# Performance work log

Measured on AMD Instinct MI355X. Metric: run time of the kernel, lower is better.

## Reference

```python
import jax, jax.numpy as jnp
import numpy as np

N_NODES = 50000
N_EDGES = 800000
ATOM_DIM = 32
EDGE_DIM = 16
HIDDEN = 64
NUM_STEPS = 3
NUM_GRAPHS = 256
OUT_DIM = 1


def setup_inputs() -> dict:
    key = jax.random.key(0)
    ks = jax.random.split(key, 20)
    s = 0.05
    inp = {
        "x": jax.random.normal(ks[0], (N_NODES, ATOM_DIM), dtype=jnp.float32),
        "edge_index": jax.random.randint(ks[1], (2, N_EDGES), 0, N_NODES),
        "edge_attr": jax.random.normal(ks[2], (N_EDGES, EDGE_DIM), dtype=jnp.float32),
        "batch": jnp.sort(jax.random.randint(ks[3], (N_NODES,), 0, NUM_GRAPHS)),
        # atom embedding
        "W_embed": jax.random.normal(ks[4], (ATOM_DIM, HIDDEN)) * s,
        "b_embed": jnp.zeros((HIDDEN,)),
        # message MLP: Linear(2H+E, H) -> ReLU -> Linear(H, H)
        "W_m1": jax.random.normal(ks[5], (2 * HIDDEN + EDGE_DIM, HIDDEN)) * s,
        "b_m1": jnp.zeros((HIDDEN,)),
        "W_m2": jax.random.normal(ks[6], (HIDDEN, HIDDEN)) * s,
        "b_m2": jnp.zeros((HIDDEN,)),
        # GRUCell (torch layout: [3H, in] stacked r,z,n)
        "W_ih": jax.random.normal(ks[7], (3 * HIDDEN, HIDDEN)) * s,
        "b_ih": jnp.zeros((3 * HIDDEN,)),
        "W_hh": jax.random.normal(ks[8], (3 * HIDDEN, HIDDEN)) * s,
        "b_hh": jnp.zeros((3 * HIDDEN,)),
        # head: Linear(2H, H) -> ReLU -> Linear(H, out)
        "W_h1": jax.random.normal(ks[9], (2 * HIDDEN, HIDDEN)) * s,
        "b_h1": jnp.zeros((HIDDEN,)),
        "W_h2": jax.random.normal(ks[10], (HIDDEN, OUT_DIM)) * s,
        "b_h2": jnp.zeros((OUT_DIM,)),
    }
    return inp


def _gru_cell(inp, h, W_ih, b_ih, W_hh, b_hh):
    gi = inp @ W_ih.T + b_ih   # [N, 3H]
    gh = h @ W_hh.T + b_hh     # [N, 3H]
    i_r, i_z, i_n = jnp.split(gi, 3, axis=-1)
    h_r, h_z, h_n = jnp.split(gh, 3, axis=-1)
    r = jax.nn.sigmoid(i_r + h_r)
    z = jax.nn.sigmoid(i_z + h_z)
    n = jnp.tanh(i_n + r * h_n)
    return (1.0 - z) * n + z * h


def reference(x, edge_index, edge_attr, batch,
              W_embed, b_embed, W_m1, b_m1, W_m2, b_m2,
              W_ih, b_ih, W_hh, b_hh, W_h1, b_h1, W_h2, b_h2):
    h = x @ W_embed + b_embed                       # [N, H]
    src, dst = edge_index[0], edge_index[1]         # PyG: x_j = x[src], x_i = x[dst]
    for _ in range(NUM_STEPS):                      # tied weights
        m = jnp.concatenate([h[src], h[dst], edge_attr], axis=-1)  # [E, 2H+ED]
        m = jax.nn.relu(m @ W_m1 + b_m1) @ W_m2 + b_m2             # [E, H]
        agg = jax.ops.segment_sum(m, dst, num_segments=N_NODES)    # scatter-add
        h = _gru_cell(agg, h, W_ih, b_ih, W_hh, b_hh)
    g_sum = jax.ops.segment_sum(h, batch, num_segments=NUM_GRAPHS)  # [G, H]
    cnt = jax.ops.segment_sum(jnp.ones((N_NODES,), h.dtype), batch,
                              num_segments=NUM_GRAPHS)
    g_mean = g_sum / jnp.maximum(cnt, 1.0)[:, None]
    g = jnp.concatenate([g_sum, g_mean], axis=-1)   # [G, 2H]
    return jax.nn.relu(g @ W_h1 + b_h1) @ W_h2 + b_h2  # [G, out]
```

## Files before the change

kernel.cpp:

```cpp
#include <hip/hip_runtime.h>
#include <math.h>

#define NN 50000
#define NE 800000
#define AD 32
#define ED 16
#define HD 64
#define NG 256
#define NTILES (NE / 16)
#define EGRID 1024
#define TPX (NTILES / 8)
#define GGRID 512
#define GTILES (NN / 16)

typedef short bf16x8 __attribute__((ext_vector_type(8)));
typedef float f32x4  __attribute__((ext_vector_type(4)));
union U4B { uint4 u; bf16x8 v; };

__device__ __forceinline__ float b2f(unsigned short s){ return __uint_as_float(((unsigned)s) << 16); }
__device__ __forceinline__ unsigned short f2bf(float f){
  unsigned u = __float_as_uint(f);
  u += 0x7fffu + ((u >> 16) & 1u);
  return (unsigned short)(u >> 16);
}
__device__ __forceinline__ unsigned packbf2(float a, float b){
  return (unsigned)f2bf(a) | ((unsigned)f2bf(b) << 16);
}
__device__ __forceinline__ bf16x8 ldfrag_g(const unsigned* p){
  U4B x; x.u = *(const uint4*)p; return x.v;
}

__global__ __launch_bounds__(256) void k_prep(const float* __restrict__ W1,
                                              const float* __restrict__ W2,
                                              const float* __restrict__ Wih,
                                              const float* __restrict__ Whh,
                                              unsigned short* __restrict__ W1Tp,
                                              unsigned short* __restrict__ W2Tp,
                                              unsigned short* __restrict__ Wgru)
{
  int idx = blockIdx.x * 256 + threadIdx.x;
  if (idx < 64 * 168){
    int n = idx / 168, k = idx % 168;
    W1Tp[idx] = (k < 144) ? f2bf(W1[k * 64 + n]) : (unsigned short)0;
    return;
  }
  idx -= 64 * 168;
  if (idx < 64 * 72){
    int n = idx / 72, k = idx % 72;
    W2Tp[idx] = (k < 64) ? f2bf(W2[k * 64 + n]) : (unsigned short)0;
    return;
  }
  idx -= 64 * 72;
  if (idx < 384 * 64){
    int j = idx & 7;
    int g = (idx >> 3) % 384;
    int blk = idx >> 3; blk /= 384;
    int q = blk & 3, ks = blk >> 2;
    int k = ks * 32 + q * 8 + j;
    float v = (g < 192) ? Wih[g * 64 + k] : Whh[(g - 192) * 64 + k];
    Wgru[idx] = f2bf(v);
  }
}

__global__ __launch_bounds__(256) void k_hist(const int* __restrict__ eidx, int* __restrict__ deg)
{
  int e = blockIdx.x * 256 + threadIdx.x;
  if (e < NE) atomicAdd(&deg[eidx[NE + e]], 1);
}

__global__ __launch_bounds__(1024) void k_scan1(const int* __restrict__ deg,
                                                int* __restrict__ cur,
                                                int* __restrict__ bsum)
{
  __shared__ int s[1024];
  const int t = threadIdx.x;
  const int idx = blockIdx.x * 1024 + t;
  int v = (idx < NN) ? deg[idx] : 0;
  s[t] = v;
  __syncthreads();
  for (int d = 1; d < 1024; d <<= 1){
    int y = (t >= d) ? s[t - d] : 0;
    __syncthreads();
    s[t] += y;
    __syncthreads();
  }
  if (idx < NN) cur[idx] = s[t] - v;
  if (t == 1023) bsum[blockIdx.x] = s[1023];
}

__global__ __launch_bounds__(64) void k_scan2(const int* __restrict__ bsum,
                                              int* __restrict__ bpre)
{
  const int t = threadIdx.x;
  const int nb = (NN + 1023) / 1024;
  int v = (t < nb) ? bsum[t] : 0;
  int orig = v;
  #pragma unroll
  for (int off = 1; off < 64; off <<= 1){
    int u = __shfl_up(v, off);
    if (t >= off) v += u;
  }
  if (t < nb) bpre[t] = v - orig;
}

__global__ __launch_bounds__(1024) void k_scan3(int* __restrict__ cur,
                                                const int* __restrict__ bpre)
{
  const int idx = blockIdx.x * 1024 + threadIdx.x;
  if (idx < NN) cur[idx] += bpre[blockIdx.x];
}

__global__ __launch_bounds__(256) void k_scatter(const int* __restrict__ eidx,
                                                 const float* __restrict__ eattr,
                                                 int* __restrict__ cur,
                                                 int* __restrict__ src_s,
                                                 int* __restrict__ dst_s,
                                                 unsigned* __restrict__ eattr_bf)
{
  int e = blockIdx.x * 256 + threadIdx.x;
  if (e >= NE) return;
  int d = eidx[NE + e];
  int p = atomicAdd(&cur[d], 1);
  src_s[p] = eidx[e];
  dst_s[p] = d;
  const float* ea = eattr + (size_t)e * 16;
  float4 v0 = *(const float4*)(ea);
  float4 v1 = *(const float4*)(ea + 4);
  float4 v2 = *(const float4*)(ea + 8);
  float4 v3 = *(const float4*)(ea + 12);
  uint4 o0, o1;
  o0.x = packbf2(v0.x, v0.y); o0.y = packbf2(v0.z, v0.w);
  o0.z = packbf2(v1.x, v1.y); o0.w = packbf2(v1.z, v1.w);
  o1.x = packbf2(v2.x, v2.y); o1.y = packbf2(v2.z, v2.w);
  o1.z = packbf2(v3.x, v3.y); o1.w = packbf2(v3.z, v3.w);
  *(uint4*)(eattr_bf + (size_t)p * 8)     = o0;
  *(uint4*)(eattr_bf + (size_t)p * 8 + 4) = o1;
}

__global__ __launch_bounds__(256) void k_embed(const float* __restrict__ x,
                                               const float* __restrict__ We,
                                               const float* __restrict__ be,
                                               float* __restrict__ h,
                                               unsigned* __restrict__ h_bf)
{
  const int t = threadIdx.x;
  const int j = t & 63, nd = t >> 6;
  const int node = blockIdx.x * 4 + nd;
  const float* xr = x + (size_t)node * AD;
  float acc = be[j];
  #pragma unroll 8
  for (int k = 0; k < AD; ++k)
    acc += xr[k] * We[k * HD + j];
  h[(size_t)node * HD + j] = acc;
  float p = __shfl_down(acc, 1);
  if (!(j & 1)) h_bf[(size_t)node * 32 + (j >> 1)] = packbf2(acc, p);
}

__global__ __launch_bounds__(256, 3) void k_edge(const unsigned* __restrict__ h_bf,
                                                 const int* __restrict__ src_s,
                                                 const int* __restrict__ dst_s,
                                                 const unsigned* __restrict__ eattr_bf,
                                                 const unsigned short* __restrict__ W1Tp,
                                                 const float* __restrict__ b1,
                                                 const unsigned* __restrict__ W2Tp32,
                                                 const float* __restrict__ b2,
                                                 float* __restrict__ agg)
{
  __shared__ __align__(16) unsigned short sW1T[64 * 168];
  __shared__ __align__(16) unsigned short sHid[4][16 * 72];

  const int t = threadIdx.x;
  {
    const uint4* srcp = (const uint4*)W1Tp;
    uint4* dstp = (uint4*)sW1T;
    for (int i = t; i < 64 * 168 * 2 / 16; i += 256) dstp[i] = srcp[i];
  }
  __syncthreads();

  const int lane = t & 63, wv = t >> 6;
  const int m = lane & 15, q = lane >> 4;

  bf16x8 w2f[4][2];
  #pragma unroll
  for (int tl = 0; tl < 4; ++tl)
    #pragma unroll
    for (int ks = 0; ks < 2; ++ks)
      w2f[tl][ks] = ldfrag_g(W2Tp32 + (tl * 16 + m) * 36 + ks * 16 + q * 4);

  float b1v[4], b2v[4];
  #pragma unroll
  for (int tl = 0; tl < 4; ++tl){ b1v[tl] = b1[tl * 16 + m]; b2v[tl] = b2[tl * 16 + m]; }

  unsigned short* sHidW = sHid[wv];

  const int xcd = blockIdx.x & 7, bi = blockIdx.x >> 3;
  const int wend = (xcd + 1) * TPX;
  const int wstep = (EGRID / 8) * 4;
  int wt = xcd * TPX + bi * 4 + wv;

  int scur = src_s[wt * 16 + m];
  int dcur = dst_s[wt * 16 + m];
  bf16x8 afc[5];
  {
    const unsigned* hs = h_bf + (size_t)scur * 32;
    const unsigned* hd = h_bf + (size_t)dcur * 32;
    afc[0] = ldfrag_g(hs + q * 4);
    afc[1] = ldfrag_g(hs + 16 + q * 4);
    afc[2] = ldfrag_g(hd + q * 4);
    afc[3] = ldfrag_g(hd + 16 + q * 4);
    if (q < 2) afc[4] = ldfrag_g(eattr_bf + (size_t)(wt * 16 + m) * 8 + q * 4);
    else { U4B x; x.u = make_uint4(0,0,0,0); afc[4] = x.v; }
  }

  while (wt < wend){
    const int wn = wt + wstep;
    const bool hasn = (wn < wend);
    int sn = 0, dn = 0;
    if (hasn){ sn = src_s[wn * 16 + m]; dn = dst_s[wn * 16 + m]; }

    f32x4 a0 = {0.f,0.f,0.f,0.f}, a1 = a0, a2 = a0, a3 = a0;
    #pragma unroll
    for (int ks = 0; ks < 5; ++ks){
      bf16x8 bb0 = *(const bf16x8*)&sW1T[( 0 + m) * 168 + ks * 32 + q * 8];
      bf16x8 bb1 = *(const bf16x8*)&sW1T[(16 + m) * 168 + ks * 32 + q * 8];
      bf16x8 bb2 = *(const bf16x8*)&sW1T[(32 + m) * 168 + ks * 32 + q * 8];
      bf16x8 bb3 = *(const bf16x8*)&sW1T[(48 + m) * 168 + ks * 32 + q * 8];
      a0 = __builtin_amdgcn_mfma_f32_16x16x32_bf16(afc[ks], bb0, a0, 0, 0, 0);
      a1 = __builtin_amdgcn_mfma_f32_16x16x32_bf16(afc[ks], bb1, a1, 0, 0, 0);
      a2 = __builtin_amdgcn_mfma_f32_16x16x32_bf16(afc[ks], bb2, a2, 0, 0, 0);
      a3 = __builtin_amdgcn_mfma_f32_16x16x32_bf16(afc[ks], bb3, a3, 0, 0, 0);
    }
    {
      f32x4 accs[4] = {a0, a1, a2, a3};
      #pragma unroll
      for (int tl = 0; tl < 4; ++tl)
        #pragma unroll
        for (int r = 0; r < 4; ++r)
          sHidW[(q * 4 + r) * 72 + tl * 16 + m] = f2bf(fmaxf(accs[tl][r] + b1v[tl], 0.f));
    }

    bf16x8 afn[5];
    if (hasn){
      const unsigned* hs = h_bf + (size_t)sn * 32;
      const unsigned* hd = h_bf + (size_t)dn * 32;
      afn[0] = ldfrag_g(hs + q * 4);
      afn[1] = ldfrag_g(hs + 16 + q * 4);
      afn[2] = ldfrag_g(hd + q * 4);
      afn[3] = ldfrag_g(hd + 16 + q * 4);
      if (q < 2) afn[4] = ldfrag_g(eattr_bf + (size_t)(wn * 16 + m) * 8 + q * 4);
      else { U4B x; x.u = make_uint4(0,0,0,0); afn[4] = x.v; }
    }

    f32x4 o0 = {0.f,0.f,0.f,0.f}, o1 = o0, o2 = o0, o3 = o0;
    #pragma unroll
    for (int ks = 0; ks < 2; ++ks){
      bf16x8 av = *(const bf16x8*)&sHidW[m * 72 + ks * 32 + q * 8];
      o0 = __builtin_amdgcn_mfma_f32_16x16x32_bf16(av, w2f[0][ks], o0, 0, 0, 0);
      o1 = __builtin_amdgcn_mfma_f32_16x16x32_bf16(av, w2f[1][ks], o1, 0, 0, 0);
      o2 = __builtin_amdgcn_mfma_f32_16x16x32_bf16(av, w2f[2][ks], o2, 0, 0, 0);
      o3 = __builtin_amdgcn_mfma_f32_16x16x32_bf16(av, w2f[3][ks], o3, 0, 0, 0);
    }

    int prev = __shfl_up(dcur, 1);
    bool isStart = (m == 0) || (dcur != prev);
    unsigned long long bal = __ballot(isStart);
    unsigned bs = (unsigned)bal & 0xFFFFu;
    int nr = __popc(bs);
    unsigned rem = bs & (bs - 1);
    int lo = 0;
    for (int r = 0; r < nr; ++r){
      int hi = rem ? (__ffs(rem) - 1) : 16;
      rem &= rem - 1;
      float s0 = 0.f, s1 = 0.f, s2 = 0.f, s3 = 0.f;
      #pragma unroll
      for (int rr = 0; rr < 4; ++rr){
        int row = q * 4 + rr;
        bool in = (row >= lo) && (row < hi);
        s0 += in ? o0[rr] : 0.f;
        s1 += in ? o1[rr] : 0.f;
        s2 += in ? o2[rr] : 0.f;
        s3 += in ? o3[rr] : 0.f;
      }
      s0 += __shfl_xor(s0, 16); s0 += __shfl_xor(s0, 32);
      s1 += __shfl_xor(s1, 16); s1 += __shfl_xor(s1, 32);
      s2 += __shfl_xor(s2, 16); s2 += __shfl_xor(s2, 32);
      s3 += __shfl_xor(s3, 16); s3 += __shfl_xor(s3, 32);
      int d = __shfl(dcur, lo);
      float cntf = (float)(hi - lo);
      if (q == 0){
        float v0 = s0 + cntf * b2v[0];
        float v1 = s1 + cntf * b2v[1];
        float v2 = s2 + cntf * b2v[2];
        float v3 = s3 + cntf * b2v[3];
        float* dp = &agg[(size_t)d * HD + m];
        if (r == 0 || r == nr - 1){
          atomicAdd(dp +  0, v0); atomicAdd(dp + 16, v1);
          atomicAdd(dp + 32, v2); atomicAdd(dp + 48, v3);
        } else {
          dp[ 0] = v0; dp[16] = v1; dp[32] = v2; dp[48] = v3;
        }
      }
      lo = hi;
    }

    wt = wn; scur = sn; dcur = dn;
    #pragma unroll
    for (int i = 0; i < 5; ++i) afc[i] = afn[i];
  }
}

__global__ __launch_bounds__(256) void k_gru(const float* __restrict__ agg,
                                             float* __restrict__ h,
                                             unsigned* __restrict__ h_bf,
                                             const unsigned short* __restrict__ Wgru,
                                             const float* __restrict__ bih,
                                             const float* __restrict__ bhh)
{
  __shared__ __align__(16) unsigned short sWg[384 * 64];
  __shared__ __align__(16) unsigned sAg[4][16 * 32];

  const int t = threadIdx.x;
  {
    const uint4* srcp = (const uint4*)Wgru;
    uint4* dstp = (uint4*)sWg;
    for (int i = t; i < 384 * 64 * 2 / 16; i += 256) dstp[i] = srcp[i];
  }
  __syncthreads();

  const int lane = t & 63, wv = t >> 6;
  const int m = lane & 15, q = lane >> 4;

  float bi_r[4], bi_z[4], bi_n[4], bh_r[4], bh_z[4], bh_n[4];
  #pragma unroll
  for (int tl = 0; tl < 4; ++tl){
    bi_r[tl] = bih[tl * 16 + m];  bi_z[tl] = bih[64 + tl * 16 + m];  bi_n[tl] = bih[128 + tl * 16 + m];
    bh_r[tl] = bhh[tl * 16 + m];  bh_z[tl] = bhh[64 + tl * 16 + m];  bh_n[tl] = bhh[128 + tl * 16 + m];
  }

  unsigned* aw = sAg[wv];

  for (int wt = blockIdx.x * 4 + wv; wt < GTILES; wt += GGRID * 4){
    const int n0 = wt * 16;

    {
      const float4* ap = (const float4*)(agg + (size_t)n0 * HD + lane * 16);
      float4 v0 = ap[0], v1 = ap[1], v2 = ap[2], v3 = ap[3];
      uint4 o0, o1;
      o0.x = packbf2(v0.x, v0.y); o0.y = packbf2(v0.z, v0.w);
      o0.z = packbf2(v1.x, v1.y); o0.w = packbf2(v1.z, v1.w);
      o1.x = packbf2(v2.x, v2.y); o1.y = packbf2(v2.z, v2.w);
      o1.z = packbf2(v3.x, v3.y); o1.w = packbf2(v3.z, v3.w);
      *(uint4*)(aw + lane * 8)     = o0;
      *(uint4*)(aw + lane * 8 + 4) = o1;
    }
    asm volatile("s_waitcnt lgkmcnt(0)" ::: "memory");

    bf16x8 aA[2], aH[2];
    #pragma unroll
    for (int ks = 0; ks < 2; ++ks){
      aA[ks] = ldfrag_g(aw + m * 32 + ks * 16 + q * 4);
      aH[ks] = ldfrag_g(h_bf + (size_t)(n0 + m) * 32 + ks * 16 + q * 4);
    }

    f32x4 ci[12], ch[12];
    #pragma unroll
    for (int tl = 0; tl < 12; ++tl){ ci[tl] = f32x4{0.f,0.f,0.f,0.f}; ch[tl] = ci[tl]; }
    #pragma unroll
    for (int ks = 0; ks < 2; ++ks){
      #pragma unroll
      for (int tl = 0; tl < 12; ++tl){
        bf16x8 bi = *(const bf16x8*)&sWg[((ks * 4 + q) * 384 + tl * 16 + m) * 8];
        ci[tl] = __builtin_amdgcn_mfma_f32_16x16x32_bf16(aA[ks], bi, ci[tl], 0, 0, 0);
        bf16x8 bh = *(const bf16x8*)&sWg[((ks * 4 + q) * 384 + 192 + tl * 16 + m) * 8];
        ch[tl] = __builtin_amdgcn_mfma_f32_16x16x32_bf16(aH[ks], bh, ch[tl], 0, 0, 0);
      }
    }

    #pragma unroll
    for (int tl = 0; tl < 4; ++tl){
      #pragma unroll
      for (int rr = 0; rr < 4; ++rr){
        const int node = n0 + q * 4 + rr;
        float ir = ci[tl][rr]     + bi_r[tl], hr = ch[tl][rr]     + bh_r[tl];
        float iz = ci[4 + tl][rr] + bi_z[tl], hz = ch[4 + tl][rr] + bh_z[tl];
        float in_ = ci[8 + tl][rr] + bi_n[tl], hn = ch[8 + tl][rr] + bh_n[tl];
        float rg = 1.f / (1.f + __expf(-(ir + hr)));
        float zg = 1.f / (1.f + __expf(-(iz + hz)));
        float ng = tanhf(in_ + rg * hn);
        float hold = h[(size_t)node * HD + tl * 16 + m];
        float hnew = (1.f - zg) * ng + zg * hold;
        h[(size_t)node * HD + tl * 16 + m] = hnew;
        float pp = __shfl_xor(hnew, 1);
        if (!(m & 1))
          h_bf[(size_t)node * 32 + tl * 8 + (m >> 1)] = packbf2(hnew, pp);
      }
    }
  }
}

__global__ __launch_bounds__(256) void k_pool(const float* __restrict__ h,
                                              const int* __restrict__ batch,
                                              float* __restrict__ gsum,
                                              float* __restrict__ cnt)
{
  const int t = threadIdx.x;
  const int j = t & 63, r = t >> 6;
  const int n0 = blockIdx.x * 64 + r * 16;
  float acc = 0.f, c = 0.f;
  int cur = -1;
  for (int i = 0; i < 16; ++i){
    int n = n0 + i;
    if (n >= NN) break;
    int g = batch[n];
    if (g != cur){
      if (cur >= 0){
        atomicAdd(&gsum[cur * HD + j], acc);
        if (j == 0) atomicAdd(&cnt[cur], c);
      }
      cur = g; acc = 0.f; c = 0.f;
    }
    acc += h[(size_t)n * HD + j];
    c += 1.f;
  }
  if (cur >= 0){
    atomicAdd(&gsum[cur * HD + j], acc);
    if (j == 0) atomicAdd(&cnt[cur], c);
  }
}

__global__ __launch_bounds__(64) void k_head(const float* __restrict__ gsum,
                                             const float* __restrict__ cnt,
                                             const float* __restrict__ W1,
                                             const float* __restrict__ b1,
                                             const float* __restrict__ W2,
                                             const float* __restrict__ b2,
                                             float* __restrict__ out)
{
  __shared__ float gv[128];
  const int g = blockIdx.x, j = threadIdx.x;
  float s = gsum[g * HD + j];
  float c = cnt[g];
  gv[j] = s;
  gv[64 + j] = s / fmaxf(c, 1.f);
  __syncthreads();
  float acc = b1[j];
  #pragma unroll 8
  for (int k = 0; k < 128; ++k)
    acc += gv[k] * W1[k * HD + j];
  acc = fmaxf(acc, 0.f);
  float v = acc * W2[j];
  #pragma unroll
  for (int off = 32; off; off >>= 1) v += __shfl_down(v, off, 64);
  if (j == 0) out[g] = v + b2[0];
}

extern "C" void kernel_launch(void* const* d_in, const int* in_sizes, int n_in,
                              void* d_out, int out_size, void* d_ws, size_t ws_size,
                              hipStream_t stream)
{
  (void)in_sizes; (void)n_in; (void)out_size; (void)ws_size;
  const float* x     = (const float*)d_in[0];
  const int*   eidx  = (const int*)d_in[1];
  const float* eattr = (const float*)d_in[2];
  const int*   batch = (const int*)d_in[3];
  const float* We    = (const float*)d_in[4];
  const float* be    = (const float*)d_in[5];
  const float* Wm1   = (const float*)d_in[6];
  const float* bm1   = (const float*)d_in[7];
  const float* Wm2   = (const float*)d_in[8];
  const float* bm2   = (const float*)d_in[9];
  const float* Wih   = (const float*)d_in[10];
  const float* bih   = (const float*)d_in[11];
  const float* Whh   = (const float*)d_in[12];
  const float* bhh   = (const float*)d_in[13];
  const float* Wh1   = (const float*)d_in[14];
  const float* bh1   = (const float*)d_in[15];
  const float* Wh2   = (const float*)d_in[16];
  const float* bh2   = (const float*)d_in[17];

  char* w = (char*)d_ws;
  float* h     = (float*)w;                      w += (size_t)NN * HD * 4;
  unsigned* h_bf = (unsigned*)w;                 w += (size_t)NN * 32 * 4;
  float* agg   = (float*)w;                      w += (size_t)NN * HD * 4;
  int*   deg   = (int*)w;                        w += (size_t)NN * 4;
  int*   cur   = (int*)w;                        w += (size_t)NN * 4;
  int*   src_s = (int*)w;                        w += (size_t)NE * 4;
  int*   dst_s = (int*)w;                        w += (size_t)NE * 4;
  unsigned* eattr_bf = (unsigned*)w;             w += (size_t)NE * 8 * 4;
  int*   bsum  = (int*)w;                        w += 64 * 4;
  int*   bpre  = (int*)w;                        w += 64 * 4;
  unsigned short* W1Tp = (unsigned short*)w;     w += 64 * 168 * 2;
  unsigned short* W2Tp = (unsigned short*)w;     w += 64 * 72 * 2;
  unsigned short* Wgru = (unsigned short*)w;     w += 384 * 64 * 2;
  float* gsum  = (float*)w;                      w += (size_t)NG * HD * 4;
  float* cnt   = (float*)w;                      w += (size_t)NG * 4;

  const int nscanb = (NN + 1023) / 1024;

  k_prep<<<156, 256, 0, stream>>>(Wm1, Wm2, Wih, Whh, W1Tp, W2Tp, Wgru);
  hipMemsetAsync(deg, 0, (size_t)NN * 4, stream);
  k_hist<<<(NE + 255) / 256, 256, 0, stream>>>(eidx, deg);
  k_scan1<<<nscanb, 1024, 0, stream>>>(deg, cur, bsum);
  k_scan2<<<1, 64, 0, stream>>>(bsum, bpre);
  k_scan3<<<nscanb, 1024, 0, stream>>>(cur, bpre);
  k_scatter<<<(NE + 255) / 256, 256, 0, stream>>>(eidx, eattr, cur, src_s, dst_s, eattr_bf);

  k_embed<<<NN / 4, 256, 0, stream>>>(x, We, be, h, h_bf);
  for (int s = 0; s < 3; ++s){
    hipMemsetAsync(agg, 0, (size_t)NN * HD * 4, stream);
    k_edge<<<EGRID, 256, 0, stream>>>(h_bf, src_s, dst_s, eattr_bf, W1Tp, bm1,
                                      (const unsigned*)W2Tp, bm2, agg);
    k_gru<<<GGRID, 256, 0, stream>>>(agg, h, h_bf, Wgru, bih, bhh);
  }
  hipMemsetAsync(gsum, 0, (size_t)(NG * HD + NG) * 4, stream);
  k_pool<<<(NN + 63) / 64, 256, 0, stream>>>(h, batch, gsum, cnt);
  k_head<<<NG, 64, 0, stream>>>(gsum, cnt, Wh1, bh1, Wh2, bh2, (float*)d_out);
}
```

Measured before the change: 710.0 us.

## Split first message layer into per-node and per-edge precomputed projections

The first message-MLP layer is linear in concat(h_src, h_dst, e), so it is decomposed into per-node projections C1=h@W1a and C2=h@W1b, computed once per step over nodes in a new k_pre kernel, plus a per-edge term E1=e@W1c+b1 computed once in k_eprep. The edge kernel then gathers the precomputed bf16 rows, adds them, applies ReLU and runs only the second GEMM. This replaces the per-edge 144-wide GEMM with a node-level GEMM, but adds a large E1 buffer (800k x 64 bf16) read every step and double rounding to bf16. The edge and GRU grid sizes also change, the GRU stops staging agg through LDS, and a fallback path is kept for when the workspace is too small.

```diff
diff --git a/kernel.cpp b/kernel.cpp
--- a/kernel.cpp
+++ b/kernel.cpp
@@ -8,16 +8,19 @@
 #define HD 64
 #define NG 256
 #define NTILES (NE / 16)
-#define EGRID 1024
+#define EGRID 1280
+#define EGRID_FB 1024
 #define TPX (NTILES / 8)
-#define GGRID 512
+#define GGRID 768
 #define GTILES (NN / 16)
+#define PGRID 782
 
 typedef short bf16x8 __attribute__((ext_vector_type(8)));
 typedef float f32x4  __attribute__((ext_vector_type(4)));
 union U4B { uint4 u; bf16x8 v; };
 
-__device__ __forceinline__ float b2f(unsigned short s){ return __uint_as_float(((unsigned)s) << 16); }
+__device__ __forceinline__ float blo(unsigned u){ return __uint_as_float(u << 16); }
+__device__ __forceinline__ float bhi(unsigned u){ return __uint_as_float(u & 0xffff0000u); }
 __device__ __forceinline__ unsigned short f2bf(float f){
   unsigned u = __float_as_uint(f);
   u += 0x7fffu + ((u >> 16) & 1u);
@@ -29,14 +32,29 @@
 __device__ __forceinline__ bf16x8 ldfrag_g(const unsigned* p){
   U4B x; x.u = *(const uint4*)p; return x.v;
 }
+__device__ __forceinline__ unsigned srp1(unsigned a, unsigned b, unsigned c){
+  float lo = fmaxf(blo(a) + blo(b) + blo(c), 0.f);
+  float hi = fmaxf(bhi(a) + bhi(b) + bhi(c), 0.f);
+  return packbf2(lo, hi);
+}
+__device__ __forceinline__ bf16x8 srp4(uint4 a, uint4 b, uint4 c){
+  U4B r;
+  r.u.x = srp1(a.x, b.x, c.x);
+  r.u.y = srp1(a.y, b.y, c.y);
+  r.u.z = srp1(a.z, b.z, c.z);
+  r.u.w = srp1(a.w, b.w, c.w);
+  return r.v;
+}
 
 __global__ __launch_bounds__(256) void k_prep(const float* __restrict__ W1,
                                               const float* __restrict__ W2,
                                               const float* __restrict__ Wih,
                                               const float* __restrict__ Whh,
+                                              const float* __restrict__ b1,
                                               unsigned short* __restrict__ W1Tp,
                                               unsigned short* __restrict__ W2Tp,
-                                              unsigned short* __restrict__ Wgru)
+                                              unsigned short* __restrict__ Wgru,
+                                              unsigned short* __restrict__ W1cTp)
 {
   int idx = blockIdx.x * 256 + threadIdx.x;
   if (idx < 64 * 168){
@@ -59,6 +77,13 @@
     int k = ks * 32 + q * 8 + j;
     float v = (g < 192) ? Wih[g * 64 + k] : Whh[(g - 192) * 64 + k];
     Wgru[idx] = f2bf(v);
+    return;
+  }
+  idx -= 384 * 64;
+  if (idx < 64 * 32){
+    int n = idx / 32, k = idx % 32;
+    float v = (k < 16) ? W1[(128 + k) * 64 + n] : (k == 16 ? b1[n] : 0.f);
+    W1cTp[idx] = f2bf(v);
   }
 }
 
@@ -137,6 +162,89 @@
   *(uint4*)(eattr_bf + (size_t)p * 8 + 4) = o1;
 }
 
+__global__ __launch_bounds__(256) void k_eprep(const unsigned* __restrict__ eattr_bf,
+                                               const unsigned* __restrict__ W1cTp32,
+                                               unsigned* __restrict__ E1)
+{
+  const int t = threadIdx.x, lane = t & 63, wv = t >> 6;
+  const int m = lane & 15, q = lane >> 4;
+  bf16x8 wf[4];
+  #pragma unroll
+  for (int tl = 0; tl < 4; ++tl)
+    wf[tl] = ldfrag_g(W1cTp32 + (tl * 16 + m) * 16 + q * 4);
+
+  for (int wt = blockIdx.x * 4 + wv; wt < NTILES; wt += 1024 * 4){
+    const int base = wt * 16;
+    U4B x;
+    if (q < 2)      x.u = *(const uint4*)(eattr_bf + (size_t)(base + m) * 8 + q * 4);
+    else if (q == 2) x.u = make_uint4(0x3F80u, 0, 0, 0);
+    else             x.u = make_uint4(0, 0, 0, 0);
+    bf16x8 a = x.v;
+    f32x4 c[4];
+    #pragma unroll
+    for (int tl = 0; tl < 4; ++tl) c[tl] = f32x4{0.f,0.f,0.f,0.f};
+    #pragma unroll
+    for (int tl = 0; tl < 4; ++tl)
+      c[tl] = __builtin_amdgcn_mfma_f32_16x16x32_bf16(a, wf[tl], c[tl], 0, 0, 0);
+    #pragma unroll
+    for (int tl = 0; tl < 4; ++tl){
+      #pragma unroll
+      for (int rr = 0; rr < 4; ++rr){
+        float v = c[tl][rr];
+        float pp = __shfl_xor(v, 1);
+        if (!(m & 1))
+          E1[(size_t)(base + q * 4 + rr) * 32 + (tl * 16 + m) / 2] = packbf2(v, pp);
+      }
+    }
+  }
+}
+
+__global__ __launch_bounds__(256, 4) void k_pre(const unsigned* __restrict__ h_bf,
+                                                const unsigned short* __restrict__ W1Tp,
+                                                unsigned* __restrict__ C12)
+{
+  const int t = threadIdx.x, lane = t & 63, wv = t >> 6;
+  const int m = lane & 15, q = lane >> 4;
+  bf16x8 wa[4][2], wb[4][2];
+  #pragma unroll
+  for (int tl = 0; tl < 4; ++tl)
+    #pragma unroll
+    for (int ks = 0; ks < 2; ++ks){
+      wa[tl][ks] = ldfrag_g((const unsigned*)(W1Tp + (tl * 16 + m) * 168 + ks * 32 + q * 8));
+      wb[tl][ks] = ldfrag_g((const unsigned*)(W1Tp + (tl * 16 + m) * 168 + 64 + ks * 32 + q * 8));
+    }
+  for (int wt = blockIdx.x * 4 + wv; wt < GTILES; wt += PGRID * 4){
+    const int n0 = wt * 16;
+    bf16x8 aH[2];
+    #pragma unroll
+    for (int ks = 0; ks < 2; ++ks)
+      aH[ks] = ldfrag_g(h_bf + (size_t)(n0 + m) * 32 + ks * 16 + q * 4);
+    f32x4 ca[4], cb[4];
+    #pragma unroll
+    for (int tl = 0; tl < 4; ++tl){ ca[tl] = f32x4{0.f,0.f,0.f,0.f}; cb[tl] = ca[tl]; }
+    #pragma unroll
+    for (int ks = 0; ks < 2; ++ks)
+      #pragma unroll
+      for (int tl = 0; tl < 4; ++tl){
+        ca[tl] = __builtin_amdgcn_mfma_f32_16x16x32_bf16(aH[ks], wa[tl][ks], ca[tl], 0, 0, 0);
+        cb[tl] = __builtin_amdgcn_mfma_f32_16x16x32_bf16(aH[ks], wb[tl][ks], cb[tl], 0, 0, 0);
+      }
+    #pragma unroll
+    for (int tl = 0; tl < 4; ++tl){
+      #pragma unroll
+      for (int rr = 0; rr < 4; ++rr){
+        const int node = n0 + q * 4 + rr;
+        float va = ca[tl][rr], vb = cb[tl][rr];
+        float pa = __shfl_xor(va, 1), pb = __shfl_xor(vb, 1);
+        if (!(m & 1)){
+          C12[(size_t)node * 64 + (tl * 16 + m) / 2]      = packbf2(va, pa);
+          C12[(size_t)node * 64 + 32 + (tl * 16 + m) / 2] = packbf2(vb, pb);
+        }
+      }
+    }
+  }
+}
+
 __global__ __launch_bounds__(256) void k_embed(const float* __restrict__ x,
                                                const float* __restrict__ We,
                                                const float* __restrict__ be,
@@ -156,27 +264,15 @@
   if (!(j & 1)) h_bf[(size_t)node * 32 + (j >> 1)] = packbf2(acc, p);
 }
 
-__global__ __launch_bounds__(256, 3) void k_edge(const unsigned* __restrict__ h_bf,
+__global__ __launch_bounds__(256, 4) void k_edge(const unsigned* __restrict__ C12,
+                                                 const unsigned* __restrict__ E1,
                                                  const int* __restrict__ src_s,
                                                  const int* __restrict__ dst_s,
-                                                 const unsigned* __restrict__ eattr_bf,
-                                                 const unsigned short* __restrict__ W1Tp,
-                                                 const float* __restrict__ b1,
                                                  const unsigned* __restrict__ W2Tp32,
                                                  const float* __restrict__ b2,
                                                  float* __restrict__ agg)
 {
-  __shared__ __align__(16) unsigned short sW1T[64 * 168];
-  __shared__ __align__(16) unsigned short sHid[4][16 * 72];
-
   const int t = threadIdx.x;
-  {
-    const uint4* srcp = (const uint4*)W1Tp;
-    uint4* dstp = (uint4*)sW1T;
-    for (int i = t; i < 64 * 168 * 2 / 16; i += 256) dstp[i] = srcp[i];
-  }
-  __syncthreads();
-
   const int lane = t & 63, wv = t >> 6;
   const int m = lane & 15, q = lane >> 4;
 
@@ -187,11 +283,9 @@
     for (int ks = 0; ks < 2; ++ks)
       w2f[tl][ks] = ldfrag_g(W2Tp32 + (tl * 16 + m) * 36 + ks * 16 + q * 4);
 
-  float b1v[4], b2v[4];
-  #pragma unroll
-  for (int tl = 0; tl < 4; ++tl){ b1v[tl] = b1[tl * 16 + m]; b2v[tl] = b2[tl * 16 + m]; }
-
-  unsigned short* sHidW = sHid[wv];
+  float b2v[4];
+  #pragma unroll
+  for (int tl = 0; tl < 4; ++tl) b2v[tl] = b2[tl * 16 + m];
 
   const int xcd = blockIdx.x & 7, bi = blockIdx.x >> 3;
   const int wend = (xcd + 1) * TPX;
@@ -200,17 +294,6 @@
 
   int scur = src_s[wt * 16 + m];
   int dcur = dst_s[wt * 16 + m];
-  bf16x8 afc[5];
-  {
-    const unsigned* hs = h_bf + (size_t)scur * 32;
-    const unsigned* hd = h_bf + (size_t)dcur * 32;
-    afc[0] = ldfrag_g(hs + q * 4);
-    afc[1] = ldfrag_g(hs + 16 + q * 4);
-    afc[2] = ldfrag_g(hd + q * 4);
-    afc[3] = ldfrag_g(hd + 16 + q * 4);
-    if (q < 2) afc[4] = ldfrag_g(eattr_bf + (size_t)(wt * 16 + m) * 8 + q * 4);
-    else { U4B x; x.u = make_uint4(0,0,0,0); afc[4] = x.v; }
-  }
 
   while (wt < wend){
     const int wn = wt + wstep;
@@ -218,48 +301,28 @@
     int sn = 0, dn = 0;
     if (hasn){ sn = src_s[wn * 16 + m]; dn = dst_s[wn * 16 + m]; }
 
-    f32x4 a0 = {0.f,0.f,0.f,0.f}, a1 = a0, a2 = a0, a3 = a0;
-    #pragma unroll
-    for (int ks = 0; ks < 5; ++ks){
-      bf16x8 bb0 = *(const bf16x8*)&sW1T[( 0 + m) * 168 + ks * 32 + q * 8];
-      bf16x8 bb1 = *(const bf16x8*)&sW1T[(16 + m) * 168 + ks * 32 + q * 8];
-      bf16x8 bb2 = *(const bf16x8*)&sW1T[(32 + m) * 168 + ks * 32 + q * 8];
-      bf16x8 bb3 = *(const bf16x8*)&sW1T[(48 + m) * 168 + ks * 32 + q * 8];
-      a0 = __builtin_amdgcn_mfma_f32_16x16x32_bf16(afc[ks], bb0, a0, 0, 0, 0);
-      a1 = __builtin_amdgcn_mfma_f32_16x16x32_bf16(afc[ks], bb1, a1, 0, 0, 0);
-      a2 = __builtin_amdgcn_mfma_f32_16x16x32_bf16(afc[ks], bb2, a2, 0, 0, 0);
-      a3 = __builtin_amdgcn_mfma_f32_16x16x32_bf16(afc[ks], bb3, a3, 0, 0, 0);
-    }
-    {
-      f32x4 accs[4] = {a0, a1, a2, a3};
-      #pragma unroll
-      for (int tl = 0; tl < 4; ++tl)
-        #pragma unroll
-        for (int r = 0; r < 4; ++r)
-          sHidW[(q * 4 + r) * 72 + tl * 16 + m] = f2bf(fmaxf(accs[tl][r] + b1v[tl], 0.f));
-    }
-
-    bf16x8 afn[5];
-    if (hasn){
-      const unsigned* hs = h_bf + (size_t)sn * 32;
-      const unsigned* hd = h_bf + (size_t)dn * 32;
-      afn[0] = ldfrag_g(hs + q * 4);
-      afn[1] = ldfrag_g(hs + 16 + q * 4);
-      afn[2] = ldfrag_g(hd + q * 4);
-      afn[3] = ldfrag_g(hd + 16 + q * 4);
-      if (q < 2) afn[4] = ldfrag_g(eattr_bf + (size_t)(wn * 16 + m) * 8 + q * 4);
-      else { U4B x; x.u = make_uint4(0,0,0,0); afn[4] = x.v; }
-    }
+    const unsigned* c1p = C12 + (size_t)scur * 64;
+    const unsigned* c2p = C12 + (size_t)dcur * 64 + 32;
+    const unsigned* e1p = E1 + (size_t)(wt * 16 + m) * 32;
+    uint4 c1a = *(const uint4*)(c1p + q * 4);
+    uint4 c1b = *(const uint4*)(c1p + 16 + q * 4);
+    uint4 c2a = *(const uint4*)(c2p + q * 4);
+    uint4 c2b = *(const uint4*)(c2p + 16 + q * 4);
+    uint4 e1a = *(const uint4*)(e1p + q * 4);
+    uint4 e1b = *(const uint4*)(e1p + 16 + q * 4);
+
+    bf16x8 af0 = srp4(c1a, c2a, e1a);
+    bf16x8 af1 = srp4(c1b, c2b, e1b);
 
     f32x4 o0 = {0.f,0.f,0.f,0.f}, o1 = o0, o2 = o0, o3 = o0;
-    #pragma unroll
-    for (int ks = 0; ks < 2; ++ks){
-      bf16x8 av = *(const bf16x8*)&sHidW[m * 72 + ks * 32 + q * 8];
-      o0 = __builtin_amdgcn_mfma_f32_16x16x32_bf16(av, w2f[0][ks], o0, 0, 0, 0);
-      o1 = __builtin_amdgcn_mfma_f32_16x16x32_bf16(av, w2f[1][ks], o1, 0, 0, 0);
-      o2 = __builtin_amdgcn_mfma_f32_16x16x32_bf16(av, w2f[2][ks], o2, 0, 0, 0);
-      o3 = __builtin_amdgcn_mfma_f32_16x16x32_bf16(av, w2f[3][ks], o3, 0, 0, 0);
-    }
+    o0 = __builtin_amdgcn_mfma_f32_16x16x32_bf16(af0, w2f[0][0], o0, 0, 0, 0);
+    o1 = __builtin_amdgcn_mfma_f32_16x16x32_bf16(af0, w2f[1][0], o1, 0, 0, 0);
+    o2 = __builtin_amdgcn_mfma_f32_16x16x32_bf16(af0, w2f[2][0], o2, 0, 0, 0);
+    o3 = __builtin_amdgcn_mfma_f32_16x16x32_bf16(af0, w2f[3][0], o3, 0, 0, 0);
+    o0 = __builtin_amdgcn_mfma_f32_16x16x32_bf16(af1, w2f[0][1], o0, 0, 0, 0);
+    o1 = __builtin_amdgcn_mfma_f32_16x16x32_bf16(af1, w2f[1][1], o1, 0, 0, 0);
+    o2 = __builtin_amdgcn_mfma_f32_16x16x32_bf16(af1, w2f[2][1], o2, 0, 0, 0);
+    o3 = __builtin_amdgcn_mfma_f32_16x16x32_bf16(af1, w2f[3][1], o3, 0, 0, 0);
 
     int prev = __shfl_up(dcur, 1);
     bool isStart = (m == 0) || (dcur != prev);
@@ -304,6 +367,157 @@
     }
 
     wt = wn; scur = sn; dcur = dn;
+  }
+}
+
+__global__ __launch_bounds__(256, 3) void k_edge_fb(const unsigned* __restrict__ h_bf,
+                                                    const int* __restrict__ src_s,
+                                                    const int* __restrict__ dst_s,
+                                                    const unsigned* __restrict__ eattr_bf,
+                                                    const unsigned short* __restrict__ W1Tp,
+                                                    const float* __restrict__ b1,
+                                                    const unsigned* __restrict__ W2Tp32,
+                                                    const float* __restrict__ b2,
+                                                    float* __restrict__ agg)
+{
+  __shared__ __align__(16) unsigned short sW1T[64 * 168];
+  __shared__ __align__(16) unsigned short sHid[4][16 * 72];
+
+  const int t = threadIdx.x;
+  {
+    const uint4* srcp = (const uint4*)W1Tp;
+    uint4* dstp = (uint4*)sW1T;
+    for (int i = t; i < 64 * 168 * 2 / 16; i += 256) dstp[i] = srcp[i];
+  }
+  __syncthreads();
+
+  const int lane = t & 63, wv = t >> 6;
+  const int m = lane & 15, q = lane >> 4;
+
+  bf16x8 w2f[4][2];
+  #pragma unroll
+  for (int tl = 0; tl < 4; ++tl)
+    #pragma unroll
+    for (int ks = 0; ks < 2; ++ks)
+      w2f[tl][ks] = ldfrag_g(W2Tp32 + (tl * 16 + m) * 36 + ks * 16 + q * 4);
+
+  float b1v[4], b2v[4];
+  #pragma unroll
+  for (int tl = 0; tl < 4; ++tl){ b1v[tl] = b1[tl * 16 + m]; b2v[tl] = b2[tl * 16 + m]; }
+
+  unsigned short* sHidW = sHid[wv];
+
+  const int xcd = blockIdx.x & 7, bi = blockIdx.x >> 3;
+  const int wend = (xcd + 1) * TPX;
+  const int wstep = (EGRID_FB / 8) * 4;
+  int wt = xcd * TPX + bi * 4 + wv;
+
+  int scur = src_s[wt * 16 + m];
+  int dcur = dst_s[wt * 16 + m];
+  bf16x8 afc[5];
+  {
+    const unsigned* hs = h_bf + (size_t)scur * 32;
+    const unsigned* hd = h_bf + (size_t)dcur * 32;
+    afc[0] = ldfrag_g(hs + q * 4);
+    afc[1] = ldfrag_g(hs + 16 + q * 4);
+    afc[2] = ldfrag_g(hd + q * 4);
+    afc[3] = ldfrag_g(hd + 16 + q * 4);
+    if (q < 2) afc[4] = ldfrag_g(eattr_bf + (size_t)(wt * 16 + m) * 8 + q * 4);
+    else { U4B x; x.u = make_uint4(0,0,0,0); afc[4] = x.v; }
+  }
+
+  while (wt < wend){
+    const int wn = wt + wstep;
+    const bool hasn = (wn < wend);
+    int sn = 0, dn = 0;
+    if (hasn){ sn = src_s[wn * 16 + m]; dn = dst_s[wn * 16 + m]; }
+
+    f32x4 a0 = {0.f,0.f,0.f,0.f}, a1 = a0, a2 = a0, a3 = a0;
+    #pragma unroll
+    for (int ks = 0; ks < 5; ++ks){
+      bf16x8 bb0 = *(const bf16x8*)&sW1T[( 0 + m) * 168 + ks * 32 + q * 8];
+      bf16x8 bb1 = *(const bf16x8*)&sW1T[(16 + m) * 168 + ks * 32 + q * 8];
+      bf16x8 bb2 = *(const bf16x8*)&sW1T[(32 + m) * 168 + ks * 32 + q * 8];
+      bf16x8 bb3 = *(const bf16x8*)&sW1T[(48 + m) * 168 + ks * 32 + q * 8];
+      a0 = __builtin_amdgcn_mfma_f32_16x16x32_bf16(afc[ks], bb0, a0, 0, 0, 0);
+      a1 = __builtin_amdgcn_mfma_f32_16x16x32_bf16(afc[ks], bb1, a1, 0, 0, 0);
+      a2 = __builtin_amdgcn_mfma_f32_16x16x32_bf16(afc[ks], bb2, a2, 0, 0, 0);
+      a3 = __builtin_amdgcn_mfma_f32_16x16x32_bf16(afc[ks], bb3, a3, 0, 0, 0);
+    }
+    {
+      f32x4 accs[4] = {a0, a1, a2, a3};
+      #pragma unroll
+      for (int tl = 0; tl < 4; ++tl)
+        #pragma unroll
+        for (int r = 0; r < 4; ++r)
+          sHidW[(q * 4 + r) * 72 + tl * 16 + m] = f2bf(fmaxf(accs[tl][r] + b1v[tl], 0.f));
+    }
+
+    bf16x8 afn[5];
+    if (hasn){
+      const unsigned* hs = h_bf + (size_t)sn * 32;
+      const unsigned* hd = h_bf + (size_t)dn * 32;
+      afn[0] = ldfrag_g(hs + q * 4);
+      afn[1] = ldfrag_g(hs + 16 + q * 4);
+      afn[2] = ldfrag_g(hd + q * 4);
+      afn[3] = ldfrag_g(hd + 16 + q * 4);
+      if (q < 2) afn[4] = ldfrag_g(eattr_bf + (size_t)(wn * 16 + m) * 8 + q * 4);
+      else { U4B x; x.u = make_uint4(0,0,0,0); afn[4] = x.v; }
+    }
+
+    f32x4 o0 = {0.f,0.f,0.f,0.f}, o1 = o0, o2 = o0, o3 = o0;
+    #pragma unroll
+    for (int ks = 0; ks < 2; ++ks){
+      bf16x8 av = *(const bf16x8*)&sHidW[m * 72 + ks * 32 + q * 8];
+      o0 = __builtin_amdgcn_mfma_f32_16x16x32_bf16(av, w2f[0][ks], o0, 0, 0, 0);
+      o1 = __builtin_amdgcn_mfma_f32_16x16x32_bf16(av, w2f[1][ks], o1, 0, 0, 0);
+      o2 = __builtin_amdgcn_mfma_f32_16x16x32_bf16(av, w2f[2][ks], o2, 0, 0, 0);
+      o3 = __builtin_amdgcn_mfma_f32_16x16x32_bf16(av, w2f[3][ks], o3, 0, 0, 0);
+    }
+
+    int prev = __shfl_up(dcur, 1);
+    bool isStart = (m == 0) || (dcur != prev);
+    unsigned long long bal = __ballot(isStart);
+    unsigned bs = (unsigned)bal & 0xFFFFu;
+    int nr = __popc(bs);
+    unsigned rem = bs & (bs - 1);
+    int lo = 0;
+    for (int r = 0; r < nr; ++r){
+      int hi = rem ? (__ffs(rem) - 1) : 16;
+      rem &= rem - 1;
+      float s0 = 0.f, s1 = 0.f, s2 = 0.f, s3 = 0.f;
+      #pragma unroll
+      for (int rr = 0; rr < 4; ++rr){
+        int row = q * 4 + rr;
+        bool in = (row >= lo) && (row < hi);
+        s0 += in ? o0[rr] : 0.f;
+        s1 += in ? o1[rr] : 0.f;
+        s2 += in ? o2[rr] : 0.f;
+        s3 += in ? o3[rr] : 0.f;
+      }
+      s0 += __shfl_xor(s0, 16); s0 += __shfl_xor(s0, 32);
+      s1 += __shfl_xor(s1, 16); s1 += __shfl_xor(s1, 32);
+      s2 += __shfl_xor(s2, 16); s2 += __shfl_xor(s2, 32);
+      s3 += __shfl_xor(s3, 16); s3 += __shfl_xor(s3, 32);
+      int d = __shfl(dcur, lo);
+      float cntf = (float)(hi - lo);
+      if (q == 0){
+        float v0 = s0 + cntf * b2v[0];
+        float v1 = s1 + cntf * b2v[1];
+        float v2 = s2 + cntf * b2v[2];
+        float v3 = s3 + cntf * b2v[3];
+        float* dp = &agg[(size_t)d * HD + m];
+        if (r == 0 || r == nr - 1){
+          atomicAdd(dp +  0, v0); atomicAdd(dp + 16, v1);
+          atomicAdd(dp + 32, v2); atomicAdd(dp + 48, v3);
+        } else {
+          dp[ 0] = v0; dp[16] = v1; dp[32] = v2; dp[48] = v3;
+        }
+      }
+      lo = hi;
+    }
+
+    wt = wn; scur = sn; dcur = dn;
     #pragma unroll
     for (int i = 0; i < 5; ++i) afc[i] = afn[i];
   }
@@ -317,7 +531,6 @@
                                              const float* __restrict__ bhh)
 {
   __shared__ __align__(16) unsigned short sWg[384 * 64];
-  __shared__ __align__(16) unsigned sAg[4][16 * 32];
 
   const int t = threadIdx.x;
   {
@@ -337,28 +550,19 @@
     bh_r[tl] = bhh[tl * 16 + m];  bh_z[tl] = bhh[64 + tl * 16 + m];  bh_n[tl] = bhh[128 + tl * 16 + m];
   }
 
-  unsigned* aw = sAg[wv];
-
   for (int wt = blockIdx.x * 4 + wv; wt < GTILES; wt += GGRID * 4){
     const int n0 = wt * 16;
 
-    {
-      const float4* ap = (const float4*)(agg + (size_t)n0 * HD + lane * 16);
-      float4 v0 = ap[0], v1 = ap[1], v2 = ap[2], v3 = ap[3];
-      uint4 o0, o1;
-      o0.x = packbf2(v0.x, v0.y); o0.y = packbf2(v0.z, v0.w);
-      o0.z = packbf2(v1.x, v1.y); o0.w = packbf2(v1.z, v1.w);
-      o1.x = packbf2(v2.x, v2.y); o1.y = packbf2(v2.z, v2.w);
-      o1.z = packbf2(v3.x, v3.y); o1.w = packbf2(v3.z, v3.w);
-      *(uint4*)(aw + lane * 8)     = o0;
-      *(uint4*)(aw + lane * 8 + 4) = o1;
-    }
-    asm volatile("s_waitcnt lgkmcnt(0)" ::: "memory");
-
     bf16x8 aA[2], aH[2];
     #pragma unroll
     for (int ks = 0; ks < 2; ++ks){
-      aA[ks] = ldfrag_g(aw + m * 32 + ks * 16 + q * 4);
+      const float* ap = agg + (size_t)(n0 + m) * 64 + ks * 32 + q * 8;
+      float4 v0 = *(const float4*)ap;
+      float4 v1 = *(const float4*)(ap + 4);
+      U4B x;
+      x.u.x = packbf2(v0.x, v0.y); x.u.y = packbf2(v0.z, v0.w);
+      x.u.z = packbf2(v1.x, v1.y); x.u.w = packbf2(v1.z, v1.w);
+      aA[ks] = x.v;
       aH[ks] = ldfrag_g(h_bf + (size_t)(n0 + m) * 32 + ks * 16 + q * 4);
     }
 
@@ -458,7 +662,7 @@
                               void* d_out, int out_size, void* d_ws, size_t ws_size,
                               hipStream_t stream)
 {
-  (void)in_sizes; (void)n_in; (void)out_size; (void)ws_size;
+  (void)in_sizes; (void)n_in; (void)out_size;
   const float* x     = (const float*)d_in[0];
   const int*   eidx  = (const int*)d_in[1];
   const float* eattr = (const float*)d_in[2];
@@ -478,7 +682,8 @@
   const float* Wh2   = (const float*)d_in[16];
   const float* bh2   = (const float*)d_in[17];
 
-  char* w = (char*)d_ws;
+  char* w0 = (char*)d_ws;
+  char* w = w0;
   float* h     = (float*)w;                      w += (size_t)NN * HD * 4;
   unsigned* h_bf = (unsigned*)w;                 w += (size_t)NN * 32 * 4;
   float* agg   = (float*)w;                      w += (size_t)NN * HD * 4;
@@ -492,24 +697,36 @@
   unsigned short* W1Tp = (unsigned short*)w;     w += 64 * 168 * 2;
   unsigned short* W2Tp = (unsigned short*)w;     w += 64 * 72 * 2;
   unsigned short* Wgru = (unsigned short*)w;     w += 384 * 64 * 2;
+  unsigned short* W1cTp = (unsigned short*)w;    w += 64 * 32 * 2;
   float* gsum  = (float*)w;                      w += (size_t)NG * HD * 4;
   float* cnt   = (float*)w;                      w += (size_t)NG * 4;
+  unsigned* C12 = (unsigned*)w;                  w += (size_t)NN * 64 * 4;
+  unsigned* E1  = (unsigned*)w;                  w += (size_t)NE * 32 * 4;
+  const bool full = ((size_t)(w - w0) <= ws_size);
 
   const int nscanb = (NN + 1023) / 1024;
 
-  k_prep<<<156, 256, 0, stream>>>(Wm1, Wm2, Wih, Whh, W1Tp, W2Tp, Wgru);
+  k_prep<<<164, 256, 0, stream>>>(Wm1, Wm2, Wih, Whh, bm1, W1Tp, W2Tp, Wgru, W1cTp);
   hipMemsetAsync(deg, 0, (size_t)NN * 4, stream);
   k_hist<<<(NE + 255) / 256, 256, 0, stream>>>(eidx, deg);
   k_scan1<<<nscanb, 1024, 0, stream>>>(deg, cur, bsum);
   k_scan2<<<1, 64, 0, stream>>>(bsum, bpre);
   k_scan3<<<nscanb, 1024, 0, stream>>>(cur, bpre);
   k_scatter<<<(NE + 255) / 256, 256, 0, stream>>>(eidx, eattr, cur, src_s, dst_s, eattr_bf);
+  if (full)
+    k_eprep<<<1024, 256, 0, stream>>>(eattr_bf, (const unsigned*)W1cTp, E1);
 
   k_embed<<<NN / 4, 256, 0, stream>>>(x, We, be, h, h_bf);
   for (int s = 0; s < 3; ++s){
     hipMemsetAsync(agg, 0, (size_t)NN * HD * 4, stream);
-    k_edge<<<EGRID, 256, 0, stream>>>(h_bf, src_s, dst_s, eattr_bf, W1Tp, bm1,
-                                      (const unsigned*)W2Tp, bm2, agg);
+    if (full){
+      k_pre<<<PGRID, 256, 0, stream>>>(h_bf, W1Tp, C12);
+      k_edge<<<EGRID, 256, 0, stream>>>(C12, E1, src_s, dst_s,
+                                        (const unsigned*)W2Tp, bm2, agg);
+    } else {
+      k_edge_fb<<<EGRID_FB, 256, 0, stream>>>(h_bf, src_s, dst_s, eattr_bf, W1Tp, bm1,
+                                              (const unsigned*)W2Tp, bm2, agg);
+    }
     k_gru<<<GGRID, 256, 0, stream>>>(agg, h, h_bf, Wgru, bih, bhh);
   }
   hipMemsetAsync(gsum, 0, (size_t)(NG * HD + NG) * 4, stream);
```

Result: faster. 578.6 us (-18.5%).
